# Kernel tuning notes

Measured on AMD Instinct MI355X. Metric: run time of the kernel, lower is better.

The kernel has to match this reference:

```python
import jax, jax.numpy as jnp
import numpy as np
import math

N_HEAD = 8
KERNEL_EPS = 1e-3   # performer-pytorch kernel_epsilon
BN_EPS = 1e-5


def _orthogonal_random_features(m, d, seed=0):
    # gaussian_orthogonal_random_matrix with scaling=0 (performer-pytorch)
    rng = np.random.default_rng(seed)
    blocks = []
    for _ in range(math.ceil(m / d)):
        q, _ = np.linalg.qr(rng.standard_normal((d, d)))
        blocks.append(q.T)
    final = np.concatenate(blocks, axis=0)[:m]
    multiplier = np.linalg.norm(rng.standard_normal((m, d)), axis=1)
    return (multiplier[:, None] * final).astype(np.float32)


def setup_inputs() -> dict:
    key = jax.random.key(0)
    ks = jax.random.split(key, 12)
    B, C, H, W = 16, 256, 56, 56
    d_head = C // N_HEAD                       # 32
    m = int(d_head * math.log(d_head))         # 110 (nb_features default)
    s = 0.02
    inp = {
        "x": jax.random.normal(ks[0], (B, C, H, W), jnp.float32),
        "bn1_gamma": jnp.ones((C,), jnp.float32),
        "bn1_beta": jnp.zeros((C,), jnp.float32),
        "bn2_gamma": jnp.ones((C,), jnp.float32),
        "bn2_beta": jnp.zeros((C,), jnp.float32),
        "Wq": jax.random.normal(ks[1], (C, C), jnp.float32) * s,
        "bq": jnp.zeros((C,), jnp.float32),
        "Wk": jax.random.normal(ks[2], (C, C), jnp.float32) * s,
        "bk": jnp.zeros((C,), jnp.float32),
        "Wv": jax.random.normal(ks[3], (C, C), jnp.float32) * s,
        "bv": jnp.zeros((C,), jnp.float32),
        "Wo": jax.random.normal(ks[4], (C, C), jnp.float32) * s,
        "bo": jnp.zeros((C,), jnp.float32),
        "proj": jnp.asarray(_orthogonal_random_features(m, d_head)),
        "conv_w": jax.random.normal(ks[5], (C, C, 3, 3), jnp.float32) * 0.02,
    }
    return inp


def _batchnorm(x, gamma, beta):
    # training-mode BatchNorm2d: batch statistics over (N, H, W)
    mean = jnp.mean(x, axis=(0, 2, 3), keepdims=True)
    var = jnp.var(x, axis=(0, 2, 3), keepdims=True)
    xn = (x - mean) * jax.lax.rsqrt(var + BN_EPS)
    return gamma[None, :, None, None] * xn + beta[None, :, None, None]


def _performer_attention(x, Wq, bq, Wk, bk, Wv, bv, Wo, bo, proj):
    # x: [B, C, H, W]; flatten spatial dims into a token sequence
    b, c, hh, ww = x.shape
    n = hh * ww
    d = c // N_HEAD
    t = x.reshape(b, c, n).transpose(0, 2, 1)  # [b, n, c]

    def split_heads(z):
        return z.reshape(b, n, N_HEAD, d).transpose(0, 2, 1, 3)  # [b, h, n, d]

    q = split_heads(t @ Wq + bq)
    k = split_heads(t @ Wk + bk)
    v = split_heads(t @ Wv + bv)

    # generalized (ReLU) kernel features, data_normalizer = d**-0.25
    norm = d ** -0.25
    phi_q = jax.nn.relu(jnp.einsum('bhnd,md->bhnm', q * norm, proj)) + KERNEL_EPS
    phi_k = jax.nn.relu(jnp.einsum('bhnd,md->bhnm', k * norm, proj)) + KERNEL_EPS

    # non-causal linear attention: O(n * m * d)
    k_sum = phi_k.sum(axis=2)                                   # [b, h, m]
    d_inv = 1.0 / jnp.einsum('bhnm,bhm->bhn', phi_q, k_sum)     # [b, h, n]
    ctx = jnp.einsum('bhnm,bhnd->bhmd', phi_k, v)               # [b, h, m, d]
    out = jnp.einsum('bhnm,bhmd->bhnd', phi_q, ctx) * d_inv[..., None]

    out = out.transpose(0, 2, 1, 3).reshape(b, n, c)            # merge heads
    out = out @ Wo + bo                                         # to_out (dropout = identity at eval)
    return out.transpose(0, 2, 1).reshape(b, c, hh, ww)


def reference(x, bn1_gamma, bn1_beta, bn2_gamma, bn2_beta,
              Wq, bq, Wk, bk, Wv, bv, Wo, bo, proj, conv_w):
    residual = x
    out = jax.nn.relu(_batchnorm(x, bn1_gamma, bn1_beta))
    out = _performer_attention(out, Wq, bq, Wk, bk, Wv, bv, Wo, bo, proj)
    out = out + x
    out = jax.nn.relu(_batchnorm(out, bn2_gamma, bn2_beta))
    out = jax.lax.conv_general_dilated(
        out, conv_w, window_strides=(1, 1), padding=((1, 1), (1, 1)),
        dimension_numbers=('NCHW', 'OIHW', 'NCHW'))
    return out + residual
```

## Files before the change

### kernel.cpp

```cpp
#include <hip/hip_runtime.h>


typedef short short8 __attribute__((ext_vector_type(8)));
typedef float f32x4 __attribute__((ext_vector_type(4)));

#define DEVI static __device__ __forceinline__

#define CDIM 256
#define SDIM 3136
#define NTOK 50176
#define NHEAD 8
#define DHEAD 32
#define MFEAT 110
#define NORMC 0.42044820762685725f
#define NPIX 50176.0f

DEVI unsigned short f2bf(float f) {
  union { float f; unsigned u; } v; v.f = f;
  unsigned r = v.u + 0x7fffu + ((v.u >> 16) & 1u);
  return (unsigned short)(r >> 16);
}

DEVI float bf2f(short h) {
  union { unsigned u; float f; } v;
  v.u = ((unsigned)(unsigned short)h) << 16;
  return v.f;
}

DEVI f32x4 mfma16(short8 a, short8 b, f32x4 c) {
  return __builtin_amdgcn_mfma_f32_16x16x32_bf16(a, b, c, 0, 0, 0);
}

DEVI unsigned long long pack4(const unsigned short* h) {
  return (unsigned long long)(h[0] | ((unsigned)h[1] << 16)) |
         ((unsigned long long)(h[2] | ((unsigned)h[3] << 16)) << 32);
}

__global__ void zero_kernel(float* p, int n) {
  for (int i = blockIdx.x * blockDim.x + threadIdx.x; i < n; i += gridDim.x * blockDim.x)
    p[i] = 0.f;
}

__global__ void prep_kernel(const float* __restrict__ Wq, const float* __restrict__ Wk,
                            const float* __restrict__ Wv, const float* __restrict__ Wo,
                            const float* __restrict__ proj, const float* __restrict__ conv_w,
                            short* __restrict__ Bqkv, short* __restrict__ WoT,
                            short* __restrict__ Bconv, short* __restrict__ projb) {
  const int t0 = blockIdx.x * blockDim.x + threadIdx.x;
  const int stride = gridDim.x * blockDim.x;
  for (int idx = t0; idx < 3 * 65536; idx += stride) {
    const int sel = idx >> 16, r = idx & 65535;
    const int ks = r >> 13, nf = (r >> 9) & 15, lane = (r >> 3) & 63, j = r & 7;
    const int n = nf * 16 + (lane & 15), k = ks * 32 + (lane >> 4) * 8 + j;
    const float* W = (sel == 0) ? Wq : ((sel == 1) ? Wk : Wv);
    Bqkv[idx] = (short)f2bf(W[k * 256 + n]);
  }
  for (int idx = t0; idx < 65536; idx += stride) {
    const int ks = idx >> 13, nf = (idx >> 9) & 15, lane = (idx >> 3) & 63, j = idx & 7;
    const int n = nf * 16 + (lane & 15), k = ks * 32 + (lane >> 4) * 8 + j;
    WoT[idx] = (short)f2bf(Wo[k * 256 + n]);
  }
  for (int idx = t0; idx < 9 * 65536; idx += stride) {
    const int off = idx >> 16, r = idx & 65535;
    const int ks = r >> 13, nf = (r >> 9) & 15, lane = (r >> 3) & 63, j = r & 7;
    const int oc = nf * 16 + (lane & 15), cin = ks * 32 + (lane >> 4) * 8 + j;
    Bconv[idx] = (short)f2bf(conv_w[(oc * 256 + cin) * 9 + off]);
  }
  for (int idx = t0; idx < 128 * 32; idx += stride) {
    const int row = idx >> 5, kk = idx & 31;
    const float v = (row < MFEAT) ? proj[row * 32 + kk] * NORMC : 0.f;
    projb[idx] = (short)f2bf(v);
  }
}

__global__ void bn_stats_kernel(const float* __restrict__ src, float* __restrict__ sums) {
  const int c = blockIdx.x & 255, b = blockIdx.x >> 8;
  const float* p = src + ((size_t)b * CDIM + c) * SDIM;
  float s = 0.f, s2 = 0.f;
  for (int i = threadIdx.x; i < SDIM; i += 256) {
    const float v = p[i];
    s += v; s2 += v * v;
  }
  for (int o = 32; o > 0; o >>= 1) { s += __shfl_down(s, o); s2 += __shfl_down(s2, o); }
  __shared__ float ls[4], ls2[4];
  const int w = threadIdx.x >> 6;
  if ((threadIdx.x & 63) == 0) { ls[w] = s; ls2[w] = s2; }
  __syncthreads();
  if (threadIdx.x == 0) {
    s = ls[0] + ls[1] + ls[2] + ls[3];
    s2 = ls2[0] + ls2[1] + ls2[2] + ls2[3];
    atomicAdd(&sums[c], s);
    atomicAdd(&sums[256 + c], s2);
  }
}

__global__ void bn_stats_nhwc(const short* __restrict__ z, float* __restrict__ sums) {
  __shared__ float L[256][16];
  const int tid = threadIdx.x;
  const int cg = tid & 31, trow = tid >> 5;
  const size_t base = (size_t)blockIdx.x * 64 * 256;
  float s[8], s2[8];
#pragma unroll
  for (int j = 0; j < 8; ++j) { s[j] = 0.f; s2[j] = 0.f; }
#pragma unroll
  for (int i = 0; i < 8; ++i) {
    const int tok = trow + i * 8;
    const short8 v = *(const short8*)&z[base + (size_t)tok * 256 + cg * 8];
#pragma unroll
    for (int j = 0; j < 8; ++j) { const float f = bf2f(v[j]); s[j] += f; s2[j] += f * f; }
  }
#pragma unroll
  for (int j = 0; j < 8; ++j) { L[tid][j] = s[j]; L[tid][8 + j] = s2[j]; }
  __syncthreads();
  const int c = tid, cgi = c >> 3, j = c & 7;
  float a = 0.f, b2 = 0.f;
#pragma unroll
  for (int tr = 0; tr < 8; ++tr) { a += L[tr * 32 + cgi][j]; b2 += L[tr * 32 + cgi][8 + j]; }
  atomicAdd(&sums[c], a);
  atomicAdd(&sums[256 + c], b2);
}

__global__ void bn_final_kernel(const float* __restrict__ sums, const float* __restrict__ gamma,
                                const float* __restrict__ beta, float* __restrict__ scsh) {
  const int c = threadIdx.x;
  const float mean = sums[c] * (1.f / NPIX);
  const float var = sums[256 + c] * (1.f / NPIX) - mean * mean;
  const float sc = gamma[c] * rsqrtf(var + 1e-5f);
  scsh[c] = sc;
  scsh[256 + c] = beta[c] - mean * sc;
}

__global__ void transpose_x(const float* __restrict__ x, const float* __restrict__ scsh,
                            short* __restrict__ dst, int mode) {
  __shared__ short T[64][72];
  const int t0 = blockIdx.x * 64;
  const int b = t0 / SDIM;
  const int s0 = t0 - b * SDIM;
  const int c0 = blockIdx.y * 64;
  const int tid = threadIdx.x;
  const int tokl = tid & 63, cl = tid >> 6;
  const float* xb = x + ((size_t)b * CDIM + c0) * SDIM + s0;
#pragma unroll
  for (int i = 0; i < 16; ++i) {
    const int c = i * 4 + cl;
    float v = xb[(size_t)c * SDIM + tokl];
    if (mode) v = fmaxf(v * scsh[c0 + c] + scsh[256 + c0 + c], 0.f);
    T[c][tokl] = (short)f2bf(v);
  }
  __syncthreads();
#pragma unroll
  for (int j = 0; j < 2; ++j) {
    const int idx = tid + j * 256;
    const int tk = idx >> 3, ch8 = idx & 7;
    unsigned short h[8];
#pragma unroll
    for (int jj = 0; jj < 8; ++jj) h[jj] = (unsigned short)T[ch8 * 8 + jj][tk];
    unsigned long long* p = (unsigned long long*)&dst[(size_t)(t0 + tk) * 256 + c0 + ch8 * 8];
    p[0] = pack4(h);
    p[1] = pack4(h + 4);
  }
}

__global__ void u2_kernel(const short* __restrict__ z, const float* __restrict__ scsh,
                          short* __restrict__ u2) {
  const int nchunks = NTOK * 32;
  for (int idx = blockIdx.x * blockDim.x + threadIdx.x; idx < nchunks;
       idx += gridDim.x * blockDim.x) {
    const int cch = idx & 31;
    const short8 v = *(const short8*)&z[(size_t)idx * 8];
    unsigned short h[8];
#pragma unroll
    for (int j = 0; j < 8; ++j) {
      const int c = cch * 8 + j;
      h[j] = f2bf(fmaxf(bf2f(v[j]) * scsh[c] + scsh[256 + c], 0.f));
    }
    unsigned long long* p = (unsigned long long*)&u2[(size_t)idx * 8];
    p[0] = pack4(h);
    p[1] = pack4(h + 4);
  }
}

__global__ __launch_bounds__(256, 4)
void qkv_gemm(const short* __restrict__ u1, const short* __restrict__ BT,
              const float* __restrict__ bq, const float* __restrict__ bk,
              const float* __restrict__ bv,
              short* __restrict__ qo, short* __restrict__ ko, short* __restrict__ vo) {
  __shared__ short A_s[64 * 256];
  const int tid = threadIdx.x;
  const int mtile = blockIdx.x, sel = blockIdx.y;
  const int token0 = mtile * 64;
  {
    const int trow = tid >> 5, cch = tid & 31;
    const short* src = u1 + (size_t)token0 * 256;
#pragma unroll
    for (int i = 0; i < 8; ++i) {
      const int tok = trow + i * 8;
      const short8 vv = *(const short8*)&src[tok * 256 + cch * 8];
      const int phys = cch ^ (tok & 31);
      *(short8*)&A_s[tok * 256 + phys * 8] = vv;
    }
  }
  __syncthreads();

  const int lane = tid & 63, wv = tid >> 6;
  const int quad = lane >> 4, l15 = lane & 15;
  const f32x4 vzero = {0.f, 0.f, 0.f, 0.f};
  f32x4 acc[4][4];
#pragma unroll
  for (int i = 0; i < 4; ++i)
#pragma unroll
    for (int j = 0; j < 4; ++j) acc[i][j] = vzero;
  const short* Bp = BT + ((size_t)sel << 16);
#pragma unroll
  for (int ks = 0; ks < 8; ++ks) {
    short8 af[4], bfr[4];
#pragma unroll
    for (int rf = 0; rf < 4; ++rf) {
      const int row = rf * 16 + l15;
      const int phys = (ks * 4 + quad) ^ (row & 31);
      af[rf] = *(const short8*)&A_s[row * 256 + phys * 8];
    }
#pragma unroll
    for (int cf = 0; cf < 4; ++cf)
      bfr[cf] = *(const short8*)&Bp[((((ks << 4) | (wv << 2) | cf) << 6) | lane) << 3];
#pragma unroll
    for (int rf = 0; rf < 4; ++rf)
#pragma unroll
      for (int cf = 0; cf < 4; ++cf)
        acc[rf][cf] = mfma16(af[rf], bfr[cf], acc[rf][cf]);
  }

  const int bb = token0 / SDIM;
  const int s0 = token0 - bb * SDIM;
#pragma unroll
  for (int cf = 0; cf < 4; ++cf) {
    const int chn = wv * 64 + cf * 16 + l15;
    const int head = chn >> 5, dd = chn & 31;
    const float bias = (sel == 0) ? bq[chn] : ((sel == 1) ? bk[chn] : bv[chn]);
#pragma unroll
    for (int rf = 0; rf < 4; ++rf) {
      const int ss = s0 + rf * 16 + quad * 4;
      if (sel < 2) {
        short* dst = (sel == 0) ? qo : ko;
        short* p = dst + ((size_t)(bb * NHEAD + head) * SDIM) * DHEAD + dd;
#pragma unroll
        for (int r = 0; r < 4; ++r)
          p[(size_t)(ss + r) * DHEAD] = (short)f2bf(acc[rf][cf][r] + bias);
      } else {
        unsigned short h4[4];
#pragma unroll
        for (int r = 0; r < 4; ++r) h4[r] = f2bf(acc[rf][cf][r] + bias);
        *(unsigned long long*)(vo + ((size_t)(bb * NHEAD + head) * DHEAD + dd) * SDIM + ss) = pack4(h4);
      }
    }
  }
}

__global__ __launch_bounds__(256, 2)
void attn_phase1(const short* __restrict__ kk, const short* __restrict__ vt,
                 const short* __restrict__ projb, float* __restrict__ ctx_acc,
                 float* __restrict__ ksum) {
  __shared__ short proj_s[128 * 40];
  __shared__ short phi_s[4][128 * 40];
  const int tid = threadIdx.x;
  const int bh = blockIdx.x >> 1, halfI = blockIdx.x & 1;
  for (int i = tid; i < 128 * 32; i += 256)
    proj_s[(i >> 5) * 40 + (i & 31)] = projb[i];
  __syncthreads();
  const int lane = tid & 63, wv = tid >> 6;
  const int quad = lane >> 4, l15 = lane & 15;
  const short* kb = kk + (size_t)bh * SDIM * DHEAD;
  const short* vb = vt + (size_t)bh * DHEAD * SDIM;
  short* myphi = phi_s[wv];
  const f32x4 vzero = {0.f, 0.f, 0.f, 0.f};
  f32x4 cacc[8][2];
  float ks_acc[8];
#pragma unroll
  for (int i = 0; i < 8; ++i) { cacc[i][0] = vzero; cacc[i][1] = vzero; ks_acc[i] = 0.f; }

  for (int ch = halfI * 4 + wv; ch < 98; ch += 8) {
    const int tok0 = ch * 32;
    short8 afr[2];
    afr[0] = *(const short8*)&kb[(size_t)(tok0 + l15) * DHEAD + quad * 8];
    afr[1] = *(const short8*)&kb[(size_t)(tok0 + 16 + l15) * DHEAD + quad * 8];
#pragma unroll
    for (int cf = 0; cf < 8; ++cf) {
      const short8 bfr = *(const short8*)&proj_s[(cf * 16 + l15) * 40 + quad * 8];
      const float epsv = (cf < 6) ? 1e-3f : ((cf == 6) ? ((l15 < 14) ? 1e-3f : 0.f) : 0.f);
#pragma unroll
      for (int fr = 0; fr < 2; ++fr) {
        f32x4 p = mfma16(afr[fr], bfr, vzero);
        unsigned short h4[4];
        float srow = 0.f;
#pragma unroll
        for (int r = 0; r < 4; ++r) {
          const float pv = fmaxf(p[r], 0.f) + epsv;
          srow += pv;
          h4[r] = f2bf(pv);
        }
        ks_acc[cf] += srow;
        *(unsigned long long*)&myphi[(cf * 16 + l15) * 40 + fr * 16 + quad * 4] = pack4(h4);
      }
    }
    short8 bv2[2];
    bv2[0] = *(const short8*)&vb[(size_t)l15 * SDIM + tok0 + quad * 8];
    bv2[1] = *(const short8*)&vb[(size_t)(16 + l15) * SDIM + tok0 + quad * 8];
#pragma unroll
    for (int mfr = 0; mfr < 8; ++mfr) {
      const short8 a2 = *(const short8*)&myphi[(mfr * 16 + l15) * 40 + quad * 8];
      cacc[mfr][0] = mfma16(a2, bv2[0], cacc[mfr][0]);
      cacc[mfr][1] = mfma16(a2, bv2[1], cacc[mfr][1]);
    }
  }
#pragma unroll
  for (int cf = 0; cf < 8; ++cf) {
    float v = ks_acc[cf];
    v += __shfl_xor(v, 16);
    v += __shfl_xor(v, 32);
    if (lane < 16) atomicAdd(&ksum[bh * 128 + cf * 16 + lane], v);
  }
  float* cb = ctx_acc + (size_t)bh * 4096;
#pragma unroll
  for (int mfr = 0; mfr < 8; ++mfr)
#pragma unroll
    for (int df = 0; df < 2; ++df)
#pragma unroll
      for (int r = 0; r < 4; ++r)
        atomicAdd(&cb[(mfr * 16 + quad * 4 + r) * 32 + df * 16 + l15], cacc[mfr][df][r]);
}

__global__ void ctx_finalize(const float* __restrict__ ctx_acc, const float* __restrict__ ksum,
                             short* __restrict__ ctx_T) {
  const int bh = blockIdx.x;
  const float* ca = ctx_acc + (size_t)bh * 4096;
  const float* ks = ksum + bh * 128;
  short* ct = ctx_T + (size_t)bh * 48 * 128;
  for (int i = threadIdx.x; i < 48 * 128; i += 256) {
    const int row = i >> 7, mf = i & 127;
    const float v = (row < 32) ? ca[mf * 32 + row] : ((row == 32) ? ks[mf] : 0.f);
    ct[i] = (short)f2bf(v);
  }
}

__global__ __launch_bounds__(256, 2)
void attn_phase2(const short* __restrict__ qq, const short* __restrict__ ctx_T,
                 const short* __restrict__ projb, short* __restrict__ Yn) {
  __shared__ short proj_s[128 * 40];
  __shared__ short ctx_s[48 * 136];
  __shared__ short phi_s[4][32 * 136];
  const int tid = threadIdx.x;
  const int bh = blockIdx.x >> 1, halfI = blockIdx.x & 1;
  for (int i = tid; i < 128 * 32; i += 256)
    proj_s[(i >> 5) * 40 + (i & 31)] = projb[i];
  {
    const short* ct = ctx_T + (size_t)bh * 48 * 128;
    for (int i = tid; i < 48 * 128; i += 256)
      ctx_s[(i >> 7) * 136 + (i & 127)] = ct[i];
  }
  __syncthreads();
  const int lane = tid & 63, wv = tid >> 6;
  const int quad = lane >> 4, l15 = lane & 15;
  const int b = bh >> 3, head = bh & 7;
  const short* qb = qq + (size_t)bh * SDIM * DHEAD;
  short* myphi = phi_s[wv];
  const f32x4 vzero = {0.f, 0.f, 0.f, 0.f};

  for (int ch = halfI * 4 + wv; ch < 98; ch += 8) {
    const int tok0 = ch * 32;
    short8 afr[2];
    afr[0] = *(const short8*)&qb[(size_t)(tok0 + l15) * DHEAD + quad * 8];
    afr[1] = *(const short8*)&qb[(size_t)(tok0 + 16 + l15) * DHEAD + quad * 8];
#pragma unroll
    for (int cf = 0; cf < 8; ++cf) {
      const short8 bfr = *(const short8*)&proj_s[(cf * 16 + l15) * 40 + quad * 8];
      const float epsv = (cf < 6) ? 1e-3f : ((cf == 6) ? ((l15 < 14) ? 1e-3f : 0.f) : 0.f);
#pragma unroll
      for (int fr = 0; fr < 2; ++fr) {
        f32x4 p = mfma16(afr[fr], bfr, vzero);
#pragma unroll
        for (int r = 0; r < 4; ++r) {
          const float pv = fmaxf(p[r], 0.f) + epsv;
          myphi[(fr * 16 + quad * 4 + r) * 136 + cf * 16 + l15] = (short)f2bf(pv);
        }
      }
    }
    f32x4 oacc[2][3];
#pragma unroll
    for (int fr = 0; fr < 2; ++fr)
#pragma unroll
      for (int c3 = 0; c3 < 3; ++c3) oacc[fr][c3] = vzero;
#pragma unroll
    for (int ksI = 0; ksI < 4; ++ksI) {
      short8 a3[2];
      a3[0] = *(const short8*)&myphi[l15 * 136 + ksI * 32 + quad * 8];
      a3[1] = *(const short8*)&myphi[(16 + l15) * 136 + ksI * 32 + quad * 8];
#pragma unroll
      for (int c3 = 0; c3 < 3; ++c3) {
        const short8 b3 = *(const short8*)&ctx_s[(c3 * 16 + l15) * 136 + ksI * 32 + quad * 8];
        oacc[0][c3] = mfma16(a3[0], b3, oacc[0][c3]);
        oacc[1][c3] = mfma16(a3[1], b3, oacc[1][c3]);
      }
    }
#pragma unroll
    for (int fr = 0; fr < 2; ++fr) {
      float dinv[4];
#pragma unroll
      for (int r = 0; r < 4; ++r) {
        const float den = __shfl(oacc[fr][2][r], quad << 4);
        dinv[r] = 1.f / den;
      }
#pragma unroll
      for (int c3 = 0; c3 < 2; ++c3)
#pragma unroll
        for (int r = 0; r < 4; ++r)
          myphi[(fr * 16 + quad * 4 + r) * 40 + c3 * 16 + l15] =
              (short)f2bf(oacc[fr][c3][r] * dinv[r]);
    }
    const size_t trow0 = (size_t)(b * SDIM + tok0) * 256 + head * 32;
#pragma unroll
    for (int it = 0; it < 2; ++it) {
      const int idx = it * 64 + lane;
      const int tl = idx >> 2, c4 = idx & 3;
      const short8 vv = *(const short8*)&myphi[tl * 40 + c4 * 8];
      *(short8*)&Yn[trow0 + (size_t)tl * 256 + c4 * 8] = vv;
    }
  }
}

__global__ __launch_bounds__(256, 4)
void wo_gemm(const short* __restrict__ Yn, const short* __restrict__ WoT,
             const float* __restrict__ bo, const short* __restrict__ xh,
             short* __restrict__ z) {
  __shared__ short A_s[64 * 264];
  const int tid = threadIdx.x;
  const int mtile = blockIdx.x;
  const int token0 = mtile * 64;
  {
    const int trow = tid >> 5, cch = tid & 31;
    const short* src = Yn + (size_t)token0 * 256;
#pragma unroll
    for (int i = 0; i < 8; ++i) {
      const int tok = trow + i * 8;
      const short8 vv = *(const short8*)&src[tok * 256 + cch * 8];
      const int phys = cch ^ (tok & 31);
      *(short8*)&A_s[tok * 256 + phys * 8] = vv;
    }
  }
  __syncthreads();

  const int lane = tid & 63, wv = tid >> 6;
  const int quad = lane >> 4, l15 = lane & 15;
  const f32x4 vzero = {0.f, 0.f, 0.f, 0.f};
  f32x4 acc[4][4];
#pragma unroll
  for (int i = 0; i < 4; ++i)
#pragma unroll
    for (int j = 0; j < 4; ++j) acc[i][j] = vzero;
#pragma unroll
  for (int ks = 0; ks < 8; ++ks) {
    short8 af[4], bfr[4];
#pragma unroll
    for (int rf = 0; rf < 4; ++rf) {
      const int row = rf * 16 + l15;
      const int phys = (ks * 4 + quad) ^ (row & 31);
      af[rf] = *(const short8*)&A_s[row * 256 + phys * 8];
    }
#pragma unroll
    for (int cf = 0; cf < 4; ++cf)
      bfr[cf] = *(const short8*)&WoT[((((ks << 4) | (wv << 2) | cf) << 6) | lane) << 3];
#pragma unroll
    for (int rf = 0; rf < 4; ++rf)
#pragma unroll
      for (int cf = 0; cf < 4; ++cf)
        acc[rf][cf] = mfma16(af[rf], bfr[cf], acc[rf][cf]);
  }
  __syncthreads();
  short* zt = A_s;
#pragma unroll
  for (int cf = 0; cf < 4; ++cf) {
    const int ocl = wv * 64 + cf * 16 + l15;
    const float bias = bo[ocl];
#pragma unroll
    for (int rf = 0; rf < 4; ++rf) {
      const int tl = rf * 16 + quad * 4;
#pragma unroll
      for (int r = 0; r < 4; ++r)
        zt[(tl + r) * 264 + ocl] = (short)f2bf(acc[rf][cf][r] + bias);
    }
  }
  __syncthreads();
#pragma unroll
  for (int j = 0; j < 8; ++j) {
    const int idx = tid + j * 256;
    const int tl = idx >> 5, ch = idx & 31;
    const short8 zv = *(const short8*)&zt[tl * 264 + ch * 8];
    const size_t gbase = (size_t)(token0 + tl) * 256 + ch * 8;
    const short8 xv = *(const short8*)&xh[gbase];
    unsigned short h[8];
#pragma unroll
    for (int jj = 0; jj < 8; ++jj) h[jj] = f2bf(bf2f(zv[jj]) + bf2f(xv[jj]));
    unsigned long long* p = (unsigned long long*)&z[gbase];
    p[0] = pack4(h);
    p[1] = pack4(h + 4);
  }
}

__global__ __launch_bounds__(256, 4)
void conv_gemm(const short* __restrict__ u2, const short* __restrict__ Bc,
               const float* __restrict__ x, float* __restrict__ out) {
  __shared__ short A_s[40 * 256];
  const int tid = threadIdx.x;
  const int bid = blockIdx.x;
  const int mtile = (bid & 7) * 196 + (bid >> 3);
  const int bb = mtile / 98, s0 = (mtile - bb * 98) * 32;
  const short* ub = u2 + (size_t)bb * SDIM * 256;
  const int lane = tid & 63, wv = tid >> 6;
  const int quad = lane >> 4, l15 = lane & 15;
  const f32x4 vzero = {0.f, 0.f, 0.f, 0.f};
  const short8 szero = {0, 0, 0, 0, 0, 0, 0, 0};
  f32x4 acc[2][4];
#pragma unroll
  for (int i = 0; i < 2; ++i)
#pragma unroll
    for (int j = 0; j < 4; ++j) acc[i][j] = vzero;

  int vy[2], vx[2];
#pragma unroll
  for (int rf = 0; rf < 2; ++rf) {
    const int so = s0 + rf * 16 + l15;
    vy[rf] = so / 56;
    vx[rf] = so - vy[rf] * 56;
  }

  short8 pref[5];
#define LOAD_DY(DYI)                                                           \
  {                                                                            \
    const int srow0 = s0 + ((DYI)-1) * 56 - 1;                                 \
    _Pragma("unroll") for (int it = 0; it < 5; ++it) {                         \
      const int chunk = tid + it * 256;                                        \
      const int idx = chunk >> 5, cchl = chunk & 31;                           \
      const int s = srow0 + idx;                                               \
      short8 vv = {0, 0, 0, 0, 0, 0, 0, 0};                                    \
      if ((unsigned)s < (unsigned)SDIM)                                        \
        vv = *(const short8*)&ub[(size_t)s * 256 + cchl * 8];                  \
      pref[it] = vv;                                                           \
    }                                                                          \
  }

  LOAD_DY(0);
#pragma unroll
  for (int dyi = 0; dyi < 3; ++dyi) {
    if (dyi) __syncthreads();
#pragma unroll
    for (int it = 0; it < 5; ++it) {
      const int chunk = tid + it * 256;
      const int idx = chunk >> 5, cchl = chunk & 31;
      const int phys = cchl ^ (idx & 31);
      *(short8*)&A_s[idx * 256 + phys * 8] = pref[it];
    }
    __syncthreads();
    if (dyi < 2) LOAD_DY(dyi + 1);
#pragma unroll
    for (int dxi = 0; dxi < 3; ++dxi) {
      const short* Bp = Bc + ((dyi * 3 + dxi) << 16);
      bool vmask[2];
#pragma unroll
      for (int rf = 0; rf < 2; ++rf)
        vmask[rf] = ((unsigned)(vy[rf] + dyi - 1) < 56u) &&
                    ((unsigned)(vx[rf] + dxi - 1) < 56u);
#pragma unroll
      for (int ks = 0; ks < 8; ++ks) {
        short8 af[2], bfr[4];
#pragma unroll
        for (int rf = 0; rf < 2; ++rf) {
          const int row = rf * 16 + l15 + dxi;
          const int phys = (ks * 4 + quad) ^ (row & 31);
          const short8 a = *(const short8*)&A_s[row * 256 + phys * 8];
          af[rf] = vmask[rf] ? a : szero;
        }
#pragma unroll
        for (int cf = 0; cf < 4; ++cf)
          bfr[cf] = *(const short8*)&Bp[((((ks << 4) | (wv << 2) | cf) << 6) | lane) << 3];
#pragma unroll
        for (int rf = 0; rf < 2; ++rf)
#pragma unroll
          for (int cf = 0; cf < 4; ++cf)
            acc[rf][cf] = mfma16(af[rf], bfr[cf], acc[rf][cf]);
      }
    }
  }
#undef LOAD_DY

#pragma unroll
  for (int cf = 0; cf < 4; ++cf) {
    const int oc = wv * 64 + cf * 16 + l15;
#pragma unroll
    for (int rf = 0; rf < 2; ++rf) {
      const int ss = s0 + rf * 16 + quad * 4;
      const size_t base = ((size_t)(bb * CDIM + oc)) * SDIM + ss;
      const f32x4 xv = *(const f32x4*)(x + base);
      f32x4 res;
#pragma unroll
      for (int r = 0; r < 4; ++r) res[r] = acc[rf][cf][r] + xv[r];
      *(f32x4*)(out + base) = res;
    }
  }
}

extern "C" void kernel_launch(void* const* d_in, const int* in_sizes, int n_in,
                              void* d_out, int out_size, void* d_ws, size_t ws_size,
                              hipStream_t stream) {
  const float* x      = (const float*)d_in[0];
  const float* bn1_g  = (const float*)d_in[1];
  const float* bn1_b  = (const float*)d_in[2];
  const float* bn2_g  = (const float*)d_in[3];
  const float* bn2_b  = (const float*)d_in[4];
  const float* Wq     = (const float*)d_in[5];
  const float* bq     = (const float*)d_in[6];
  const float* Wk     = (const float*)d_in[7];
  const float* bk     = (const float*)d_in[8];
  const float* Wv     = (const float*)d_in[9];
  const float* bv     = (const float*)d_in[10];
  const float* Wo     = (const float*)d_in[11];
  const float* bo     = (const float*)d_in[12];
  const float* proj   = (const float*)d_in[13];
  const float* conv_w = (const float*)d_in[14];
  float* out = (float*)d_out;
  char* ws = (char*)d_ws;

  const size_t OFF_K     = 0;
  const size_t OFF_V     = 25690112;
  const size_t OFF_BQKV  = 51380224;
  const size_t OFF_WOT   = 51773440;
  const size_t OFF_BCONV = 51904512;
  const size_t OFF_PROJB = 53084160;
  const size_t OFF_CTXA  = 53092352;
  const size_t OFF_KSUM  = 55189504;
  const size_t OFF_BN1S  = 55255040;
  const size_t OFF_BN2S  = 55257088;
  const size_t OFF_SC1   = 55259136;
  const size_t OFF_SC2   = 55261184;
  const size_t OFF_CTXT  = 55263232;
  const size_t WS_NEEDED = 56836096;

  if (ws_size < WS_NEEDED) {
    zero_kernel<<<2048, 256, 0, stream>>>(out, out_size);
    return;
  }

  short* qb    = (short*)d_out;
  short* half2 = (short*)d_out + 12845056;
  short* kb    = (short*)(ws + OFF_K);
  short* vtb   = (short*)(ws + OFF_V);
  short* Yn    = (short*)(ws + OFF_K);
  short* zbuf  = (short*)(ws + OFF_V);
  short* u2b   = (short*)(ws + OFF_K);
  short* Bqkv  = (short*)(ws + OFF_BQKV);
  short* WoT   = (short*)(ws + OFF_WOT);
  short* Bconv = (short*)(ws + OFF_BCONV);
  short* projb = (short*)(ws + OFF_PROJB);
  float* ctxa  = (float*)(ws + OFF_CTXA);
  float* ksum  = (float*)(ws + OFF_KSUM);
  float* bn1s  = (float*)(ws + OFF_BN1S);
  float* bn2s  = (float*)(ws + OFF_BN2S);
  float* sc1   = (float*)(ws + OFF_SC1);
  float* sc2   = (float*)(ws + OFF_SC2);
  short* ctxT  = (short*)(ws + OFF_CTXT);

  zero_kernel<<<512, 256, 0, stream>>>(ctxa, (2097152 + 65536 + 2048 + 2048) / 4);
  prep_kernel<<<256, 256, 0, stream>>>(Wq, Wk, Wv, Wo, proj, conv_w, Bqkv, WoT, Bconv, projb);
  bn_stats_kernel<<<4096, 256, 0, stream>>>(x, bn1s);
  bn_final_kernel<<<1, 256, 0, stream>>>(bn1s, bn1_g, bn1_b, sc1);
  transpose_x<<<dim3(784, 4), 256, 0, stream>>>(x, sc1, half2, 1);
  qkv_gemm<<<dim3(784, 3), 256, 0, stream>>>(half2, Bqkv, bq, bk, bv, qb, kb, vtb);
  attn_phase1<<<256, 256, 0, stream>>>(kb, vtb, projb, ctxa, ksum);
  ctx_finalize<<<128, 256, 0, stream>>>(ctxa, ksum, ctxT);
  attn_phase2<<<256, 256, 0, stream>>>(qb, ctxT, projb, Yn);
  transpose_x<<<dim3(784, 4), 256, 0, stream>>>(x, sc1, half2, 0);
  wo_gemm<<<784, 256, 0, stream>>>(Yn, WoT, bo, half2, zbuf);
  bn_stats_nhwc<<<784, 256, 0, stream>>>(zbuf, bn2s);
  bn_final_kernel<<<1, 256, 0, stream>>>(bn2s, bn2_g, bn2_b, sc2);
  u2_kernel<<<1024, 256, 0, stream>>>(zbuf, sc2, u2b);
  conv_gemm<<<1568, 256, 0, stream>>>(u2b, Bconv, x, out);
}
```

Measured before the change: 500.7 us.

## Fuse BN2 stats into wo_gemm and BN2+ReLU into conv loads; drop ctx_finalize

Accumulates BN2 channel sums inside the wo_gemm epilogue, removing the separate bn_stats_nhwc pass. BN2 scale/shift plus ReLU is applied while conv_gemm loads its input tiles, which eliminates the u2 intermediate buffer and its kernel. The ctx_finalize conversion moves into attn_phase2's shared-memory load. This removes several full passes over a 25MB activation and three launches, at the cost of extra ALU work in the conv loads, which are repeated per dy row.

```diff
diff --git a/kernel.cpp b/kernel.cpp
--- a/kernel.cpp
+++ b/kernel.cpp
@@ -94,32 +94,6 @@
   }
 }
 
-__global__ void bn_stats_nhwc(const short* __restrict__ z, float* __restrict__ sums) {
-  __shared__ float L[256][16];
-  const int tid = threadIdx.x;
-  const int cg = tid & 31, trow = tid >> 5;
-  const size_t base = (size_t)blockIdx.x * 64 * 256;
-  float s[8], s2[8];
-#pragma unroll
-  for (int j = 0; j < 8; ++j) { s[j] = 0.f; s2[j] = 0.f; }
-#pragma unroll
-  for (int i = 0; i < 8; ++i) {
-    const int tok = trow + i * 8;
-    const short8 v = *(const short8*)&z[base + (size_t)tok * 256 + cg * 8];
-#pragma unroll
-    for (int j = 0; j < 8; ++j) { const float f = bf2f(v[j]); s[j] += f; s2[j] += f * f; }
-  }
-#pragma unroll
-  for (int j = 0; j < 8; ++j) { L[tid][j] = s[j]; L[tid][8 + j] = s2[j]; }
-  __syncthreads();
-  const int c = tid, cgi = c >> 3, j = c & 7;
-  float a = 0.f, b2 = 0.f;
-#pragma unroll
-  for (int tr = 0; tr < 8; ++tr) { a += L[tr * 32 + cgi][j]; b2 += L[tr * 32 + cgi][8 + j]; }
-  atomicAdd(&sums[c], a);
-  atomicAdd(&sums[256 + c], b2);
-}
-
 __global__ void bn_final_kernel(const float* __restrict__ sums, const float* __restrict__ gamma,
                                 const float* __restrict__ beta, float* __restrict__ scsh) {
   const int c = threadIdx.x;
@@ -156,25 +130,6 @@
 #pragma unroll
     for (int jj = 0; jj < 8; ++jj) h[jj] = (unsigned short)T[ch8 * 8 + jj][tk];
     unsigned long long* p = (unsigned long long*)&dst[(size_t)(t0 + tk) * 256 + c0 + ch8 * 8];
-    p[0] = pack4(h);
-    p[1] = pack4(h + 4);
-  }
-}
-
-__global__ void u2_kernel(const short* __restrict__ z, const float* __restrict__ scsh,
-                          short* __restrict__ u2) {
-  const int nchunks = NTOK * 32;
-  for (int idx = blockIdx.x * blockDim.x + threadIdx.x; idx < nchunks;
-       idx += gridDim.x * blockDim.x) {
-    const int cch = idx & 31;
-    const short8 v = *(const short8*)&z[(size_t)idx * 8];
-    unsigned short h[8];
-#pragma unroll
-    for (int j = 0; j < 8; ++j) {
-      const int c = cch * 8 + j;
-      h[j] = f2bf(fmaxf(bf2f(v[j]) * scsh[c] + scsh[256 + c], 0.f));
-    }
-    unsigned long long* p = (unsigned long long*)&u2[(size_t)idx * 8];
     p[0] = pack4(h);
     p[1] = pack4(h + 4);
   }
@@ -329,22 +284,10 @@
         atomicAdd(&cb[(mfr * 16 + quad * 4 + r) * 32 + df * 16 + l15], cacc[mfr][df][r]);
 }
 
-__global__ void ctx_finalize(const float* __restrict__ ctx_acc, const float* __restrict__ ksum,
-                             short* __restrict__ ctx_T) {
-  const int bh = blockIdx.x;
-  const float* ca = ctx_acc + (size_t)bh * 4096;
-  const float* ks = ksum + bh * 128;
-  short* ct = ctx_T + (size_t)bh * 48 * 128;
-  for (int i = threadIdx.x; i < 48 * 128; i += 256) {
-    const int row = i >> 7, mf = i & 127;
-    const float v = (row < 32) ? ca[mf * 32 + row] : ((row == 32) ? ks[mf] : 0.f);
-    ct[i] = (short)f2bf(v);
-  }
-}
-
 __global__ __launch_bounds__(256, 2)
-void attn_phase2(const short* __restrict__ qq, const short* __restrict__ ctx_T,
-                 const short* __restrict__ projb, short* __restrict__ Yn) {
+void attn_phase2(const short* __restrict__ qq, const float* __restrict__ ctx_acc,
+                 const float* __restrict__ ksum, const short* __restrict__ projb,
+                 short* __restrict__ Yn) {
   __shared__ short proj_s[128 * 40];
   __shared__ short ctx_s[48 * 136];
   __shared__ short phi_s[4][32 * 136];
@@ -353,9 +296,13 @@
   for (int i = tid; i < 128 * 32; i += 256)
     proj_s[(i >> 5) * 40 + (i & 31)] = projb[i];
   {
-    const short* ct = ctx_T + (size_t)bh * 48 * 128;
-    for (int i = tid; i < 48 * 128; i += 256)
-      ctx_s[(i >> 7) * 136 + (i & 127)] = ct[i];
+    const float* ca = ctx_acc + (size_t)bh * 4096;
+    const float* ks = ksum + bh * 128;
+    for (int i = tid; i < 48 * 128; i += 256) {
+      const int row = i >> 7, mf = i & 127;
+      const float v = (row < 32) ? ca[mf * 32 + row] : ((row == 32) ? ks[mf] : 0.f);
+      ctx_s[row * 136 + mf] = (short)f2bf(v);
+    }
   }
   __syncthreads();
   const int lane = tid & 63, wv = tid >> 6;
@@ -430,7 +377,7 @@
 __global__ __launch_bounds__(256, 4)
 void wo_gemm(const short* __restrict__ Yn, const short* __restrict__ WoT,
              const float* __restrict__ bo, const short* __restrict__ xh,
-             short* __restrict__ z) {
+             short* __restrict__ z, float* __restrict__ sums) {
   __shared__ short A_s[64 * 264];
   const int tid = threadIdx.x;
   const int mtile = blockIdx.x;
@@ -489,6 +436,9 @@
     }
   }
   __syncthreads();
+  float s[8], s2[8];
+#pragma unroll
+  for (int j = 0; j < 8; ++j) { s[j] = 0.f; s2[j] = 0.f; }
 #pragma unroll
   for (int j = 0; j < 8; ++j) {
     const int idx = tid + j * 256;
@@ -498,22 +448,41 @@
     const short8 xv = *(const short8*)&xh[gbase];
     unsigned short h[8];
 #pragma unroll
-    for (int jj = 0; jj < 8; ++jj) h[jj] = f2bf(bf2f(zv[jj]) + bf2f(xv[jj]));
+    for (int jj = 0; jj < 8; ++jj) {
+      h[jj] = f2bf(bf2f(zv[jj]) + bf2f(xv[jj]));
+      const float f = bf2f((short)h[jj]);
+      s[jj] += f; s2[jj] += f * f;
+    }
     unsigned long long* p = (unsigned long long*)&z[gbase];
     p[0] = pack4(h);
     p[1] = pack4(h + 4);
   }
+  __syncthreads();
+  float* L = (float*)A_s;
+#pragma unroll
+  for (int j = 0; j < 8; ++j) { L[tid * 16 + j] = s[j]; L[tid * 16 + 8 + j] = s2[j]; }
+  __syncthreads();
+  const int c = tid, cgi = c >> 3, j2 = c & 7;
+  float a = 0.f, b2 = 0.f;
+#pragma unroll
+  for (int tr = 0; tr < 8; ++tr) {
+    a += L[(tr * 32 + cgi) * 16 + j2];
+    b2 += L[(tr * 32 + cgi) * 16 + 8 + j2];
+  }
+  atomicAdd(&sums[c], a);
+  atomicAdd(&sums[256 + c], b2);
 }
 
 __global__ __launch_bounds__(256, 4)
-void conv_gemm(const short* __restrict__ u2, const short* __restrict__ Bc,
-               const float* __restrict__ x, float* __restrict__ out) {
+void conv_gemm(const short* __restrict__ zin, const float* __restrict__ scsh,
+               const short* __restrict__ Bc, const float* __restrict__ x,
+               float* __restrict__ out) {
   __shared__ short A_s[40 * 256];
   const int tid = threadIdx.x;
   const int bid = blockIdx.x;
   const int mtile = (bid & 7) * 196 + (bid >> 3);
   const int bb = mtile / 98, s0 = (mtile - bb * 98) * 32;
-  const short* ub = u2 + (size_t)bb * SDIM * 256;
+  const short* ub = zin + (size_t)bb * SDIM * 256;
   const int lane = tid & 63, wv = tid >> 6;
   const int quad = lane >> 4, l15 = lane & 15;
   const f32x4 vzero = {0.f, 0.f, 0.f, 0.f};
@@ -523,6 +492,14 @@
   for (int i = 0; i < 2; ++i)
 #pragma unroll
     for (int j = 0; j < 4; ++j) acc[i][j] = vzero;
+
+  const int cch = tid & 31;
+  float sc_r[8], sh_r[8];
+#pragma unroll
+  for (int j = 0; j < 8; ++j) {
+    sc_r[j] = scsh[cch * 8 + j];
+    sh_r[j] = scsh[256 + cch * 8 + j];
+  }
 
   int vy[2], vx[2];
 #pragma unroll
@@ -538,11 +515,17 @@
     const int srow0 = s0 + ((DYI)-1) * 56 - 1;                                 \
     _Pragma("unroll") for (int it = 0; it < 5; ++it) {                         \
       const int chunk = tid + it * 256;                                        \
-      const int idx = chunk >> 5, cchl = chunk & 31;                           \
+      const int idx = chunk >> 5;                                              \
       const int s = srow0 + idx;                                               \
       short8 vv = {0, 0, 0, 0, 0, 0, 0, 0};                                    \
-      if ((unsigned)s < (unsigned)SDIM)                                        \
-        vv = *(const short8*)&ub[(size_t)s * 256 + cchl * 8];                  \
+      if ((unsigned)s < (unsigned)SDIM) {                                      \
+        const short8 raw = *(const short8*)&ub[(size_t)s * 256 + cch * 8];     \
+        unsigned short hh[8];                                                  \
+        _Pragma("unroll") for (int jj = 0; jj < 8; ++jj)                       \
+            hh[jj] = f2bf(fmaxf(bf2f(raw[jj]) * sc_r[jj] + sh_r[jj], 0.f));    \
+        _Pragma("unroll") for (int jj = 0; jj < 8; ++jj)                       \
+            vv[jj] = (short)hh[jj];                                            \
+      }                                                                        \
       pref[it] = vv;                                                           \
     }                                                                          \
   }
@@ -554,8 +537,8 @@
 #pragma unroll
     for (int it = 0; it < 5; ++it) {
       const int chunk = tid + it * 256;
-      const int idx = chunk >> 5, cchl = chunk & 31;
-      const int phys = cchl ^ (idx & 31);
+      const int idx = chunk >> 5;
+      const int phys = cch ^ (idx & 31);
       *(short8*)&A_s[idx * 256 + phys * 8] = pref[it];
     }
     __syncthreads();
@@ -640,7 +623,6 @@
   const size_t OFF_BN2S  = 55257088;
   const size_t OFF_SC1   = 55259136;
   const size_t OFF_SC2   = 55261184;
-  const size_t OFF_CTXT  = 55263232;
   const size_t WS_NEEDED = 56836096;
 
   if (ws_size < WS_NEEDED) {
@@ -654,7 +636,6 @@
   short* vtb   = (short*)(ws + OFF_V);
   short* Yn    = (short*)(ws + OFF_K);
   short* zbuf  = (short*)(ws + OFF_V);
-  short* u2b   = (short*)(ws + OFF_K);
   short* Bqkv  = (short*)(ws + OFF_BQKV);
   short* WoT   = (short*)(ws + OFF_WOT);
   short* Bconv = (short*)(ws + OFF_BCONV);
@@ -665,7 +646,6 @@
   float* bn2s  = (float*)(ws + OFF_BN2S);
   float* sc1   = (float*)(ws + OFF_SC1);
   float* sc2   = (float*)(ws + OFF_SC2);
-  short* ctxT  = (short*)(ws + OFF_CTXT);
 
   zero_kernel<<<512, 256, 0, stream>>>(ctxa, (2097152 + 65536 + 2048 + 2048) / 4);
   prep_kernel<<<256, 256, 0, stream>>>(Wq, Wk, Wv, Wo, proj, conv_w, Bqkv, WoT, Bconv, projb);
@@ -674,12 +654,9 @@
   transpose_x<<<dim3(784, 4), 256, 0, stream>>>(x, sc1, half2, 1);
   qkv_gemm<<<dim3(784, 3), 256, 0, stream>>>(half2, Bqkv, bq, bk, bv, qb, kb, vtb);
   attn_phase1<<<256, 256, 0, stream>>>(kb, vtb, projb, ctxa, ksum);
-  ctx_finalize<<<128, 256, 0, stream>>>(ctxa, ksum, ctxT);
-  attn_phase2<<<256, 256, 0, stream>>>(qb, ctxT, projb, Yn);
+  attn_phase2<<<256, 256, 0, stream>>>(qb, ctxa, ksum, projb, Yn);
   transpose_x<<<dim3(784, 4), 256, 0, stream>>>(x, sc1, half2, 0);
-  wo_gemm<<<784, 256, 0, stream>>>(Yn, WoT, bo, half2, zbuf);
-  bn_stats_nhwc<<<784, 256, 0, stream>>>(zbuf, bn2s);
+  wo_gemm<<<784, 256, 0, stream>>>(Yn, WoT, bo, half2, zbuf, bn2s);
   bn_final_kernel<<<1, 256, 0, stream>>>(bn2s, bn2_g, bn2_b, sc2);
-  u2_kernel<<<1024, 256, 0, stream>>>(zbuf, sc2, u2b);
-  conv_gemm<<<1568, 256, 0, stream>>>(u2b, Bconv, x, out);
-}
+  conv_gemm<<<1568, 256, 0, stream>>>(zbuf, sc2, Bconv, x, out);
+}
```

Result: slower. 516.6 us (+3.2%).
